# Kernel tuning notes

Hardware: AMD Instinct MI355X
Metric: run time of the kernel (lower is better)

## Reference

```python
import jax, jax.numpy as jnp
import numpy as np

N = 65536   # number of feature vectors (feat_num)
D = 512     # feature dim (feat_size)
NC = 256    # number of unique classes n; N % NC == 0 as required by feat.chunk(n, 0)
EPS = 1e-8  # torch nn.CosineSimilarity eps


def setup_inputs() -> dict:
    key = jax.random.key(0)
    feat = jax.random.normal(key, (N, D), dtype=jnp.float32)
    # contiguous class blocks so chunk(n,0) groups match unique labels (module's implicit assumption)
    label = (jnp.arange(N, dtype=jnp.int32) // (N // NC)).astype(jnp.int32)
    return {"feat": feat, "label": label}


def reference(feat, label):
    n = NC  # len(label.unique()); static by construction
    # per-class centers: mean of each contiguous chunk  -> [n, D]
    centers = feat.reshape(n, N // n, D).mean(axis=1)
    # pairwise cosine similarity (torch CosineSimilarity: dot / (max(|x|,eps)*max(|y|,eps)))
    norms = jnp.sqrt(jnp.sum(centers * centers, axis=1, keepdims=True))  # [n,1]
    normed = centers / jnp.maximum(norms, EPS)
    sim = normed @ normed.T  # [n, n]
    # mask = label1 eq label1^T; labels are unique -> identity mask. Off-diagonal min per row.
    eye = jnp.eye(n, dtype=bool)
    dist_an = jnp.min(jnp.where(eye, jnp.inf, sim), axis=1)  # [n]
    # sum_i (1 - min_j!=i sim[i,j])
    return jnp.sum(1.0 - dist_an)
```

## Files before the change

kernel.cpp:

```cpp
#include <hip/hip_runtime.h>
#include <math.h>

#define NFEAT 65536
#define DIM   512
#define D4    128
#define NCLS  256
#define ROWS_PER_CLASS 256
#define SPLIT 8
#define EPSV  1e-8f

__global__ __launch_bounds__(256)
void k1_partial(const float4* __restrict__ feat4, float4* __restrict__ partial4) {
    const int b    = blockIdx.x;
    const int cls  = b >> 2;
    const int qtr  = b & 3;
    const int t    = threadIdx.x;
    const int col4 = t & 127;
    const int sub  = t >> 7;
    const int row0 = cls * ROWS_PER_CLASS + qtr * 64 + sub * 32;

    const float4* p = feat4 + (size_t)row0 * D4 + col4;
    float4 acc = make_float4(0.f, 0.f, 0.f, 0.f);
#pragma unroll 8
    for (int r = 0; r < 32; ++r) {
        float4 v = p[(size_t)r * D4];
        acc.x += v.x; acc.y += v.y; acc.z += v.z; acc.w += v.w;
    }
    const int sp = qtr * 2 + sub;
    partial4[((size_t)cls * SPLIT + sp) * D4 + col4] = acc;
}

__global__ __launch_bounds__(128)
void k2_normalize(const float4* __restrict__ partial4, float4* __restrict__ nT4) {
    const int cls = blockIdx.x;
    const int t   = threadIdx.x;

    float4 acc = make_float4(0.f, 0.f, 0.f, 0.f);
#pragma unroll
    for (int p = 0; p < SPLIT; ++p) {
        float4 v = partial4[((size_t)cls * SPLIT + p) * D4 + t];
        acc.x += v.x; acc.y += v.y; acc.z += v.z; acc.w += v.w;
    }
    const float ms = 1.0f / (float)ROWS_PER_CLASS;
    acc.x *= ms; acc.y *= ms; acc.z *= ms; acc.w *= ms;

    float ss = acc.x*acc.x + acc.y*acc.y + acc.z*acc.z + acc.w*acc.w;
#pragma unroll
    for (int o = 32; o > 0; o >>= 1) ss += __shfl_down(ss, o, 64);

    __shared__ float wsum[2];
    __shared__ float s_inv;
    if ((t & 63) == 0) wsum[t >> 6] = ss;
    __syncthreads();
    if (t == 0) {
        float nrm = sqrtf(wsum[0] + wsum[1]);
        s_inv = 1.0f / fmaxf(nrm, EPSV);
    }
    __syncthreads();
    const float inv = s_inv;
    acc.x *= inv; acc.y *= inv; acc.z *= inv; acc.w *= inv;
    nT4[(size_t)t * NCLS + cls] = acc;
}

__global__ __launch_bounds__(256)
void k3_colmin(const float4* __restrict__ nT4, float* __restrict__ row_vals) {
    const int j = blockIdx.x;
    const int i = threadIdx.x;

    __shared__ float4 bj[D4];
    if (i < D4) bj[i] = nT4[(size_t)i * NCLS + j];
    __syncthreads();

    float acc = 0.f;
#pragma unroll 8
    for (int g = 0; g < D4; ++g) {
        float4 a = nT4[(size_t)g * NCLS + i];
        float4 b = bj[g];
        acc += a.x*b.x + a.y*b.y + a.z*b.z + a.w*b.w;
    }
    if (i == j) acc = INFINITY;

#pragma unroll
    for (int o = 32; o > 0; o >>= 1) acc = fminf(acc, __shfl_down(acc, o, 64));

    __shared__ float wmin[4];
    if ((i & 63) == 0) wmin[i >> 6] = acc;
    __syncthreads();
    if (i == 0) {
        float m = fminf(fminf(wmin[0], wmin[1]), fminf(wmin[2], wmin[3]));
        row_vals[j] = 1.0f - m;
    }
}

__global__ __launch_bounds__(256)
void k4_sum(const float* __restrict__ row_vals, float* __restrict__ out) {
    const int t = threadIdx.x;
    float v = row_vals[t];
#pragma unroll
    for (int o = 32; o > 0; o >>= 1) v += __shfl_down(v, o, 64);
    __shared__ float wsum[4];
    if ((t & 63) == 0) wsum[t >> 6] = v;
    __syncthreads();
    if (t == 0) out[0] = wsum[0] + wsum[1] + wsum[2] + wsum[3];
}

extern "C" void kernel_launch(void* const* d_in, const int* in_sizes, int n_in,
                              void* d_out, int out_size, void* d_ws, size_t ws_size,
                              hipStream_t stream) {
    const float* feat = (const float*)d_in[0];
    float* out = (float*)d_out;

    float* ws       = (float*)d_ws;
    float* partial  = ws;
    float* nT4f     = partial + (size_t)NCLS * SPLIT * DIM;
    float* row_vals = nT4f + (size_t)NCLS * DIM;

    k1_partial   <<<NCLS * 4, 256, 0, stream>>>((const float4*)feat, (float4*)partial);
    k2_normalize <<<NCLS,     128, 0, stream>>>((const float4*)partial, (float4*)nT4f);
    k3_colmin    <<<NCLS,     256, 0, stream>>>((const float4*)nT4f, row_vals);
    k4_sum       <<<1,        256, 0, stream>>>(row_vals, out);
}
```

Baseline: 202.9 us.

## Fuse center reduction with normalization and min with sum via atomics

Merges the partial-sum and normalize kernels into one 1024-thread block per class that reduces its rows through shared memory. It also folds the final sum into the min kernel with an atomicAdd on the output, which block 0 of the first kernel zeroes. This cuts four launches to two and drops the partial-buffer round trip. In exchange the grid for the bandwidth-bound 128 MB read shrinks from 1024 blocks to 256 larger ones, and the float atomic accumulation order is nondeterministic.

Result: no change. 199.9 us (-1.4%).

```diff
diff --git a/kernel.cpp b/kernel.cpp
--- a/kernel.cpp
+++ b/kernel.cpp
@@ -6,18 +6,16 @@
 #define D4    128
 #define NCLS  256
 #define ROWS_PER_CLASS 256
-#define SPLIT 8
 #define EPSV  1e-8f
 
-__global__ __launch_bounds__(256)
-void k1_partial(const float4* __restrict__ feat4, float4* __restrict__ partial4) {
-    const int b    = blockIdx.x;
-    const int cls  = b >> 2;
-    const int qtr  = b & 3;
+__global__ __launch_bounds__(1024)
+void kA_center_norm(const float4* __restrict__ feat4, float4* __restrict__ nT4,
+                    float* __restrict__ out) {
+    const int cls  = blockIdx.x;
     const int t    = threadIdx.x;
     const int col4 = t & 127;
     const int sub  = t >> 7;
-    const int row0 = cls * ROWS_PER_CLASS + qtr * 64 + sub * 32;
+    const int row0 = cls * ROWS_PER_CLASS + sub * 32;
 
     const float4* p = feat4 + (size_t)row0 * D4 + col4;
     float4 acc = make_float4(0.f, 0.f, 0.f, 0.f);
@@ -26,44 +24,45 @@
         float4 v = p[(size_t)r * D4];
         acc.x += v.x; acc.y += v.y; acc.z += v.z; acc.w += v.w;
     }
-    const int sp = qtr * 2 + sub;
-    partial4[((size_t)cls * SPLIT + sp) * D4 + col4] = acc;
-}
 
-__global__ __launch_bounds__(128)
-void k2_normalize(const float4* __restrict__ partial4, float4* __restrict__ nT4) {
-    const int cls = blockIdx.x;
-    const int t   = threadIdx.x;
-
-    float4 acc = make_float4(0.f, 0.f, 0.f, 0.f);
-#pragma unroll
-    for (int p = 0; p < SPLIT; ++p) {
-        float4 v = partial4[((size_t)cls * SPLIT + p) * D4 + t];
-        acc.x += v.x; acc.y += v.y; acc.z += v.z; acc.w += v.w;
-    }
-    const float ms = 1.0f / (float)ROWS_PER_CLASS;
-    acc.x *= ms; acc.y *= ms; acc.z *= ms; acc.w *= ms;
-
-    float ss = acc.x*acc.x + acc.y*acc.y + acc.z*acc.z + acc.w*acc.w;
-#pragma unroll
-    for (int o = 32; o > 0; o >>= 1) ss += __shfl_down(ss, o, 64);
+    __shared__ float4 red[1024];
+    red[t] = acc;
+    __syncthreads();
 
     __shared__ float wsum[2];
     __shared__ float s_inv;
-    if ((t & 63) == 0) wsum[t >> 6] = ss;
+    float4 c = make_float4(0.f, 0.f, 0.f, 0.f);
+    if (t < 128) {
+        c = red[t];
+#pragma unroll
+        for (int s = 1; s < 8; ++s) {
+            float4 v = red[t + 128 * s];
+            c.x += v.x; c.y += v.y; c.z += v.z; c.w += v.w;
+        }
+        const float ms = 1.0f / (float)ROWS_PER_CLASS;
+        c.x *= ms; c.y *= ms; c.z *= ms; c.w *= ms;
+
+        float ss = c.x*c.x + c.y*c.y + c.z*c.z + c.w*c.w;
+#pragma unroll
+        for (int o = 32; o > 0; o >>= 1) ss += __shfl_down(ss, o, 64);
+        if ((t & 63) == 0) wsum[t >> 6] = ss;
+    }
     __syncthreads();
     if (t == 0) {
         float nrm = sqrtf(wsum[0] + wsum[1]);
         s_inv = 1.0f / fmaxf(nrm, EPSV);
+        if (cls == 0) out[0] = 0.f;
     }
     __syncthreads();
-    const float inv = s_inv;
-    acc.x *= inv; acc.y *= inv; acc.z *= inv; acc.w *= inv;
-    nT4[(size_t)t * NCLS + cls] = acc;
+    if (t < 128) {
+        const float inv = s_inv;
+        c.x *= inv; c.y *= inv; c.z *= inv; c.w *= inv;
+        nT4[(size_t)col4 * NCLS + cls] = c;
+    }
 }
 
 __global__ __launch_bounds__(256)
-void k3_colmin(const float4* __restrict__ nT4, float* __restrict__ row_vals) {
+void kB_min_sum(const float4* __restrict__ nT4, float* __restrict__ out) {
     const int j = blockIdx.x;
     const int i = threadIdx.x;
 
@@ -88,20 +87,8 @@
     __syncthreads();
     if (i == 0) {
         float m = fminf(fminf(wmin[0], wmin[1]), fminf(wmin[2], wmin[3]));
-        row_vals[j] = 1.0f - m;
+        atomicAdd(out, 1.0f - m);
     }
-}
-
-__global__ __launch_bounds__(256)
-void k4_sum(const float* __restrict__ row_vals, float* __restrict__ out) {
-    const int t = threadIdx.x;
-    float v = row_vals[t];
-#pragma unroll
-    for (int o = 32; o > 0; o >>= 1) v += __shfl_down(v, o, 64);
-    __shared__ float wsum[4];
-    if ((t & 63) == 0) wsum[t >> 6] = v;
-    __syncthreads();
-    if (t == 0) out[0] = wsum[0] + wsum[1] + wsum[2] + wsum[3];
 }
 
 extern "C" void kernel_launch(void* const* d_in, const int* in_sizes, int n_in,
@@ -110,13 +97,8 @@
     const float* feat = (const float*)d_in[0];
     float* out = (float*)d_out;
 
-    float* ws       = (float*)d_ws;
-    float* partial  = ws;
-    float* nT4f     = partial + (size_t)NCLS * SPLIT * DIM;
-    float* row_vals = nT4f + (size_t)NCLS * DIM;
+    float* nT4f = (float*)d_ws;
 
-    k1_partial   <<<NCLS * 4, 256, 0, stream>>>((const float4*)feat, (float4*)partial);
-    k2_normalize <<<NCLS,     128, 0, stream>>>((const float4*)partial, (float4*)nT4f);
-    k3_colmin    <<<NCLS,     256, 0, stream>>>((const float4*)nT4f, row_vals);
-    k4_sum       <<<1,        256, 0, stream>>>(row_vals, out);
+    kA_center_norm <<<NCLS, 1024, 0, stream>>>((const float4*)feat, (float4*)nT4f, out);
+    kB_min_sum     <<<NCLS,  256, 0, stream>>>((const float4*)nT4f, out);
 }
```
